# Kernel tuning notes

Hardware: AMD Instinct MI355X
Metric: run time of the kernel (lower is better)

## Reference

```python
import jax, jax.numpy as jnp
import numpy as np

B, C, D, O = 4, 4096, 1024, 1024
PROJ = 256
RANKS = [1, 2, 4, 8]
E = len(RANKS)
CLAMP_MAX = float(np.log(1.0 / 0.01))  # log(100)


def setup_inputs() -> dict:
    key = jax.random.key(0)
    ks = jax.random.split(key, 16)
    inp = {
        "x": jax.random.normal(ks[0], (B, C, D), dtype=jnp.float32),
        "W": jax.random.normal(ks[1], (O, D), dtype=jnp.float32) / np.sqrt(D),
        "Wp": jax.random.normal(ks[2], (PROJ, D), dtype=jnp.float32) / np.sqrt(D),
        "bp": jnp.zeros((PROJ,), dtype=jnp.float32),
        "sim": jax.random.normal(ks[3], (PROJ, E), dtype=jnp.float32) * 0.01,
        "temp": jnp.full((1,), np.log(1.0 / 0.5), dtype=jnp.float32),
    }
    for i, r in enumerate(RANKS):
        inp[f"Wd{i}"] = jax.random.normal(ks[4 + 2 * i], (r, D), dtype=jnp.float32) / r
        inp[f"Wu{i}"] = jax.random.normal(ks[5 + 2 * i], (O, r), dtype=jnp.float32) * 0.01
    return inp


def _l2norm(v, axis):
    return v / jnp.maximum(jnp.linalg.norm(v, axis=axis, keepdims=True), 1e-12)


def reference(x, W, Wp, bp, sim, temp, Wd0, Wu0, Wd1, Wu1, Wd2, Wu2, Wd3, Wu3):
    # base linear (bias=False)
    base = jnp.einsum("bcd,od->bco", x, W)

    # cosine top-k gate on flattened tokens
    xf = x.reshape(-1, x.shape[-1])                         # [N, D]
    proj = _l2norm(xf @ Wp.T + bp, axis=1)                  # [N, PROJ]
    simn = _l2norm(sim, axis=0)                             # [PROJ, E]
    scale = jnp.exp(jnp.minimum(temp, CLAMP_MAX))
    logits = (proj @ simn) * scale                          # [N, E]

    # eval mode: no noise. softmax then top-1 mask * prob
    lw = jax.nn.softmax(logits, axis=1)
    top1 = jnp.argmax(lw, axis=1)                           # [N]
    ret = jnp.where(jnp.arange(E)[None, :] == top1[:, None], lw, 0.0)
    ret = ret.reshape(x.shape[0], x.shape[1], E)            # [B, C, E]

    # dense per-expert LoRA (ranks differ, so small fixed loop)
    downs = (Wd0, Wd1, Wd2, Wd3)
    ups = (Wu0, Wu1, Wu2, Wu3)
    l = jnp.stack(
        [jnp.einsum("bcr,or->bco", jnp.einsum("bcd,rd->bcr", x, d), u)
         for d, u in zip(downs, ups)],
        axis=2,
    )                                                       # [B, C, E, O]
    res = jnp.sum(ret[..., None] * l, axis=2)               # [B, C, O]
    return base + res
```

## Files before the change

### kernel.cpp

```cpp
#include <hip/hip_runtime.h>

#define TOK 16384
#define DD 1024
#define OO 1024
#define KE 1088
#define NT 17
#define NB1 288
#define CLAMPV 4.605170185988091f

typedef __attribute__((ext_vector_type(8))) short short8;
typedef __attribute__((ext_vector_type(4))) float f32x4;

__device__ __forceinline__ unsigned short f2bf(float f) {
  unsigned int u = __float_as_uint(f);
  return (unsigned short)((u + 0x7FFFu + ((u >> 16) & 1u)) >> 16);
}

__device__ __forceinline__ void gload16(const unsigned short* g, unsigned short* l) {
  __builtin_amdgcn_global_load_lds(
      (const __attribute__((address_space(1))) void*)g,
      (__attribute__((address_space(3))) void*)l, 16, 0, 0);
}

__device__ __forceinline__ float down_val(int j, int d,
    const float* __restrict__ Wd0, const float* __restrict__ Wd1,
    const float* __restrict__ Wd2, const float* __restrict__ Wd3) {
  if (j == 0) return Wd0[d];
  if (j < 3) return Wd1[(j - 1) * DD + d];
  if (j < 7) return Wd2[(j - 3) * DD + d];
  if (j < 15) return Wd3[(j - 7) * DD + d];
  return 0.f;
}

__global__ __launch_bounds__(256) void prep3(
    const float* __restrict__ W, const float* __restrict__ Wp,
    const float* __restrict__ sim, const float* __restrict__ bp,
    const float* __restrict__ Wd0, const float* __restrict__ Wd1,
    const float* __restrict__ Wd2, const float* __restrict__ Wd3,
    const float* __restrict__ Wu0, const float* __restrict__ Wu1,
    const float* __restrict__ Wu2, const float* __restrict__ Wu3,
    unsigned short* __restrict__ Bx, unsigned short* __restrict__ B1,
    unsigned short* __restrict__ Ax, float* __restrict__ v4,
    float* __restrict__ c4) {
  __shared__ float simn_l[256][4];
  __shared__ float part[4][4];
  const int tid = threadIdx.x;
  if (blockIdx.x < 4) {
    float4 sv = *(const float4*)&sim[tid * 4];
    float v[4] = {sv.x * sv.x, sv.y * sv.y, sv.z * sv.z, sv.w * sv.w};
#pragma unroll
    for (int off = 1; off < 64; off <<= 1) {
#pragma unroll
      for (int e = 0; e < 4; ++e) v[e] += __shfl_xor(v[e], off, 64);
    }
    int wv = tid >> 6, ln = tid & 63;
    if (ln == 0) { part[wv][0] = v[0]; part[wv][1] = v[1]; part[wv][2] = v[2]; part[wv][3] = v[3]; }
    __syncthreads();
    float n0 = fmaxf(sqrtf(part[0][0] + part[1][0] + part[2][0] + part[3][0]), 1e-12f);
    float n1 = fmaxf(sqrtf(part[0][1] + part[1][1] + part[2][1] + part[3][1]), 1e-12f);
    float n2 = fmaxf(sqrtf(part[0][2] + part[1][2] + part[2][2] + part[3][2]), 1e-12f);
    float n3 = fmaxf(sqrtf(part[0][3] + part[1][3] + part[2][3] + part[3][3]), 1e-12f);
    simn_l[tid][0] = sv.x / n0; simn_l[tid][1] = sv.y / n1;
    simn_l[tid][2] = sv.z / n2; simn_l[tid][3] = sv.w / n3;
    __syncthreads();
    int d = blockIdx.x * 256 + tid;
    float a0 = 0.f, a1 = 0.f, a2 = 0.f, a3 = 0.f;
    for (int j = 0; j < 256; ++j) {
      float w = Wp[j * DD + d];
      a0 = __builtin_fmaf(w, simn_l[j][0], a0);
      a1 = __builtin_fmaf(w, simn_l[j][1], a1);
      a2 = __builtin_fmaf(w, simn_l[j][2], a2);
      a3 = __builtin_fmaf(w, simn_l[j][3], a3);
    }
    v4[d] = a0; v4[1024 + d] = a1; v4[2048 + d] = a2; v4[3072 + d] = a3;
    if (blockIdx.x == 0) {
      float bpv = bp[tid];
      float pc[4] = {simn_l[tid][0] * bpv, simn_l[tid][1] * bpv,
                     simn_l[tid][2] * bpv, simn_l[tid][3] * bpv};
#pragma unroll
      for (int off = 1; off < 64; off <<= 1) {
#pragma unroll
        for (int e = 0; e < 4; ++e) pc[e] += __shfl_xor(pc[e], off, 64);
      }
      __syncthreads();
      if (ln == 0) { part[wv][0] = pc[0]; part[wv][1] = pc[1]; part[wv][2] = pc[2]; part[wv][3] = pc[3]; }
      __syncthreads();
      if (tid == 0) {
#pragma unroll
        for (int e = 0; e < 4; ++e)
          c4[e] = part[0][e] + part[1][e] + part[2][e] + part[3][e];
      }
    }
  }
  const int nB1 = NB1 * DD;
  const int nWb = OO * KE;
  const int nXpad = TOK * 48;
  const int total = nB1 + nWb + nXpad;
  for (int i = blockIdx.x * 256 + tid; i < total; i += gridDim.x * 256) {
    if (i < nB1) {
      int r = i >> 10, c = i & 1023;
      float v = 0.f;
      if (r < 256) v = Wp[r * DD + c];
      else if (r < 271) v = down_val(r - 256, c, Wd0, Wd1, Wd2, Wd3);
      B1[i] = f2bf(v);
    } else if (i < nB1 + nWb) {
      int j = i - nB1;
      int o = j / KE, c = j - o * KE;
      float v = 0.f;
      if (c < 1024) v = W[o * DD + c];
      else if (c == 1024) v = Wu0[o];
      else if (c < 1027) v = Wu1[o * 2 + (c - 1025)];
      else if (c < 1031) v = Wu2[o * 4 + (c - 1027)];
      else if (c < 1039) v = Wu3[o * 8 + (c - 1031)];
      Bx[j] = f2bf(v);
    } else {
      int j = i - nB1 - nWb;
      int row = j / 48, c = j - row * 48;
      Ax[row * KE + 1040 + c] = 0;
    }
  }
}

__global__ __launch_bounds__(256, 2) void gemm2f(
    const float* __restrict__ x, const float* __restrict__ v4,
    unsigned short* __restrict__ Ax, const unsigned short* __restrict__ B1,
    const float* __restrict__ c4, const float* __restrict__ bp,
    const float* __restrict__ temp) {
  __shared__ __align__(16) unsigned short as1[2][32 * 32];
  __shared__ __align__(16) unsigned short bs1[2][NB1 * 32];
  __shared__ float ssq_s[2][32];
  __shared__ float xdown_s[32][16];
  __shared__ __align__(16) float dots_s[32][4];
  const int tid = threadIdx.x;
  const int lane = tid & 63, wv = tid >> 6;
  const int wm = wv >> 1, wn = wv & 1;
  const int r0 = blockIdx.x * 32;
  const int ro = lane & 15, ko = (lane >> 4) * 8;
  const int srow = lane >> 2, scol = (lane & 3) * 8;
  const int xr = tid >> 3;
  const int xc = (tid & 7) * 4;
  const float* xgp = &x[(r0 + xr) * DD + xc];
  unsigned short* axp = &Ax[(r0 + xr) * KE + xc];
  f32x4 acc[9] = {};
  float dotp[4] = {};

#define STB1(KT, BUF)                                                         \
  for (int c = wv; c < 18; c += 4)                                            \
    gload16(&B1[(c * 16 + srow) * DD + (KT) * 32 + scol], &bs1[BUF][c * 512]);

#define XSTG(KT, BUF) do {                                                    \
    float4 xv = *(const float4*)(xgp + (KT) * 32);                            \
    float4 va = *(const float4*)&v4[(KT) * 32 + xc];                          \
    float4 vb = *(const float4*)&v4[1024 + (KT) * 32 + xc];                   \
    float4 vc = *(const float4*)&v4[2048 + (KT) * 32 + xc];                   \
    float4 vd = *(const float4*)&v4[3072 + (KT) * 32 + xc];                   \
    dotp[0] = __builtin_fmaf(xv.x, va.x, __builtin_fmaf(xv.y, va.y,           \
              __builtin_fmaf(xv.z, va.z, __builtin_fmaf(xv.w, va.w, dotp[0])))); \
    dotp[1] = __builtin_fmaf(xv.x, vb.x, __builtin_fmaf(xv.y, vb.y,           \
              __builtin_fmaf(xv.z, vb.z, __builtin_fmaf(xv.w, vb.w, dotp[1])))); \
    dotp[2] = __builtin_fmaf(xv.x, vc.x, __builtin_fmaf(xv.y, vc.y,           \
              __builtin_fmaf(xv.z, vc.z, __builtin_fmaf(xv.w, vc.w, dotp[2])))); \
    dotp[3] = __builtin_fmaf(xv.x, vd.x, __builtin_fmaf(xv.y, vd.y,           \
              __builtin_fmaf(xv.z, vd.z, __builtin_fmaf(xv.w, vd.w, dotp[3])))); \
    union { unsigned short s[4]; uint2 q; } pk;                               \
    pk.s[0] = f2bf(xv.x); pk.s[1] = f2bf(xv.y);                               \
    pk.s[2] = f2bf(xv.z); pk.s[3] = f2bf(xv.w);                               \
    *reinterpret_cast<uint2*>(axp + (KT) * 32) = pk.q;                        \
    *reinterpret_cast<uint2*>(&as1[BUF][xr * 32 + xc]) = pk.q;                \
  } while (0)

#define MM(BUF) do {                                                          \
    const unsigned short* ap = &as1[BUF][0];                                  \
    const unsigned short* bpp = &bs1[BUF][0];                                 \
    short8 af = *reinterpret_cast<const short8*>(ap + (wm * 16 + ro) * 32 + ko); \
    _Pragma("unroll")                                                         \
    for (int n = 0; n < 9; ++n) {                                             \
      short8 bf = *reinterpret_cast<const short8*>(                           \
          bpp + (wn * 144 + n * 16 + ro) * 32 + ko);                          \
      acc[n] = __builtin_amdgcn_mfma_f32_16x16x32_bf16(af, bf, acc[n], 0, 0, 0); \
    }                                                                         \
  } while (0)

  XSTG(0, 0);
  STB1(0, 0)
  __syncthreads();
  int cur = 0;
  for (int u = 0; u < 32; ++u) {
    if (u < 31) {
      XSTG(u + 1, cur ^ 1);
      STB1(u + 1, cur ^ 1)
    }
    MM(cur);
    if (u < 31) {
      __syncthreads();
      cur ^= 1;
    }
  }

#pragma unroll
  for (int off = 1; off < 8; off <<= 1) {
#pragma unroll
    for (int e = 0; e < 4; ++e) dotp[e] += __shfl_xor(dotp[e], off, 64);
  }
  if ((lane & 7) == 0) {
    dots_s[xr][0] = dotp[0]; dots_s[xr][1] = dotp[1];
    dots_s[xr][2] = dotp[2]; dots_s[xr][3] = dotp[3];
  }

  float ssqp[4] = {};
#pragma unroll
  for (int n = 0; n < 9; ++n) {
    int col = wn * 144 + n * 16 + ro;
    if (col < 256) {
      float b = bp[col];
#pragma unroll
      for (int r = 0; r < 4; ++r) {
        float a = acc[n][r] + b;
        ssqp[r] = __builtin_fmaf(a, a, ssqp[r]);
      }
    }
  }
#pragma unroll
  for (int off = 1; off < 16; off <<= 1) {
#pragma unroll
    for (int r = 0; r < 4; ++r) ssqp[r] += __shfl_xor(ssqp[r], off, 64);
  }
  if (ro == 0) {
#pragma unroll
    for (int r = 0; r < 4; ++r)
      ssq_s[wn][wm * 16 + (lane >> 4) * 4 + r] = ssqp[r];
  }
  if (wn == 1 && ro < 15) {
#pragma unroll
    for (int r = 0; r < 4; ++r)
      xdown_s[wm * 16 + (lane >> 4) * 4 + r][ro] = acc[7][r];
  }
  __syncthreads();

  if (tid < 32) {
    const int row = tid, t = r0 + row;
    float ssqT = ssq_s[0][row] + ssq_s[1][row];
    float4 cc = *reinterpret_cast<const float4*>(c4);
    float scale = expf(fminf(temp[0], CLAMPV));
    float inv = scale / fmaxf(sqrtf(ssqT), 1e-12f);
    float l[4];
    l[0] = (dots_s[row][0] + cc.x) * inv; l[1] = (dots_s[row][1] + cc.y) * inv;
    l[2] = (dots_s[row][2] + cc.z) * inv; l[3] = (dots_s[row][3] + cc.w) * inv;
    int be = 0; float m = l[0];
    if (l[1] > m) { m = l[1]; be = 1; }
    if (l[2] > m) { m = l[2]; be = 2; }
    if (l[3] > m) { m = l[3]; be = 3; }
    float den = expf(l[0] - m) + expf(l[1] - m) + expf(l[2] - m) + expf(l[3] - m);
    float g = 1.0f / den;
    int off = (1 << be) - 1;
    int rr = 1 << be;
    union { unsigned short s[16]; uint4 v[2]; } o;
#pragma unroll
    for (int j = 0; j < 16; ++j) {
      float dv = xdown_s[row][j & 15];
      float v = (j >= off && j < off + rr) ? g * dv : 0.f;
      o.s[j] = f2bf(v);
    }
    uint4* dst = reinterpret_cast<uint4*>(&Ax[t * KE + 1024]);
    dst[0] = o.v[0];
    dst[1] = o.v[1];
  }
#undef STB1
#undef XSTG
#undef MM
}

__global__ __launch_bounds__(512, 2) void main_gemm8(
    const unsigned short* __restrict__ A, const unsigned short* __restrict__ Bm,
    float* __restrict__ C) {
  __shared__ __align__(16) unsigned short lbuf[2][32768];
  const int tid = threadIdx.x;
  const int lane = tid & 63, wv = tid >> 6;
  const int wm = wv >> 2, wn = wv & 3;
  const int dd = blockIdx.x;
  const int tt = (dd & 7) * 32 + (dd >> 3);
  const int bx = tt & 3, by = tt >> 2;
  const int r0 = by * 256, c0 = bx * 256;
  const int ro = lane & 15, ko = (lane >> 4) * 8;
  const int rowb = ro * 128;
  const int swz = (ro & 7) << 4;
  const int lk0 = (ko * 2) ^ swz;
  const int lk1 = (64 + ko * 2) ^ swz;
  const int ll = (lane * 16) ^ ((lane >> 3) << 4);
  const int sro = ll >> 7;
  const int sk = (ll & 127) >> 1;
  f32x4 acc[8][4] = {};
  short8 Af[4][2], B0[2][2], B1r[2][2];

#define STG(MTX, GRB, HBU, BUF, U2)                                           \
  do {                                                                        \
    gload16(&MTX[((GRB) + (0 * 8 + wv) * 8 + sro) * KE + (U2) * 64 + sk],     \
            &lbuf[BUF][(HBU) + (0 * 8 + wv) * 512]);                          \
    gload16(&MTX[((GRB) + (1 * 8 + wv) * 8 + sro) * KE + (U2) * 64 + sk],     \
            &lbuf[BUF][(HBU) + (1 * 8 + wv) * 512]);                          \
  } while (0)

#define LDA(FI, QM, LK) (*reinterpret_cast<const short8*>(                    \
    (const char*)Ab + wm * 16384 + (QM) * 8192 + (FI) * 2048 + rowb + (LK)))
#define LDB(FN, QN, LK) (*reinterpret_cast<const short8*>(                    \
    (const char*)Bb + wn * 8192 + (QN) * 4096 + (FN) * 2048 + rowb + (LK)))

#define MMQ(QM, QN, BF)                                                       \
  do {                                                                        \
    _Pragma("unroll")                                                         \
    for (int fi = 0; fi < 4; ++fi) {                                          \
      _Pragma("unroll")                                                       \
      for (int fn = 0; fn < 2; ++fn) {                                        \
        acc[(QM)*4+fi][(QN)*2+fn] = __builtin_amdgcn_mfma_f32_16x16x32_bf16(  \
            Af[fi][0], BF[fn][0], acc[(QM)*4+fi][(QN)*2+fn], 0, 0, 0);        \
        acc[(QM)*4+fi][(QN)*2+fn] = __builtin_amdgcn_mfma_f32_16x16x32_bf16(  \
            Af[fi][1], BF[fn][1], acc[(QM)*4+fi][(QN)*2+fn], 0, 0, 0);        \
      }                                                                       \
    }                                                                         \
  } while (0)

  STG(Bm, c0,       16384, 0, 0);
  STG(A,  r0,       0,     0, 0);
  STG(Bm, c0 + 128, 24576, 0, 0);
  STG(A,  r0 + 128, 8192,  0, 0);
  STG(Bm, c0,       16384, 1, 1);
  STG(A,  r0,       0,     1, 1);
  asm volatile("s_waitcnt vmcnt(4)" ::: "memory");
  __builtin_amdgcn_s_barrier();

  for (int u = 0; u < NT; ++u) {
    const int db = u & 1;
    const unsigned short* Ab = &lbuf[db][0];
    const unsigned short* Bb = &lbuf[db][16384];
#pragma unroll
    for (int fi = 0; fi < 4; ++fi) { Af[fi][0] = LDA(fi, 0, lk0); Af[fi][1] = LDA(fi, 0, lk1); }
#pragma unroll
    for (int fn = 0; fn < 2; ++fn) { B0[fn][0] = LDB(fn, 0, lk0); B0[fn][1] = LDB(fn, 0, lk1); }
    if (u + 1 < NT) STG(Bm, c0 + 128, 24576, (u + 1) & 1, u + 1);
    __builtin_amdgcn_s_barrier();
    __builtin_amdgcn_s_setprio(1);
    MMQ(0, 0, B0);
    __builtin_amdgcn_s_setprio(0);
    __builtin_amdgcn_s_barrier();
#pragma unroll
    for (int fn = 0; fn < 2; ++fn) { B1r[fn][0] = LDB(fn, 1, lk0); B1r[fn][1] = LDB(fn, 1, lk1); }
    if (u + 1 < NT) STG(A, r0 + 128, 8192, (u + 1) & 1, u + 1);
    __builtin_amdgcn_s_barrier();
    __builtin_amdgcn_s_setprio(1);
    MMQ(0, 1, B1r);
    __builtin_amdgcn_s_setprio(0);
    __builtin_amdgcn_s_barrier();
#pragma unroll
    for (int fi = 0; fi < 4; ++fi) { Af[fi][0] = LDA(fi, 1, lk0); Af[fi][1] = LDA(fi, 1, lk1); }
    if (u + 2 < NT) STG(Bm, c0, 16384, db, u + 2);
    __builtin_amdgcn_s_barrier();
    __builtin_amdgcn_s_setprio(1);
    MMQ(1, 1, B1r);
    __builtin_amdgcn_s_setprio(0);
    __builtin_amdgcn_s_barrier();
    if (u + 2 < NT) STG(A, r0, 0, db, u + 2);
    __builtin_amdgcn_s_barrier();
    __builtin_amdgcn_s_setprio(1);
    MMQ(1, 0, B0);
    __builtin_amdgcn_s_setprio(0);
    if (u + 2 < NT) {
      asm volatile("s_waitcnt vmcnt(4)" ::: "memory");
    } else if (u == NT - 2) {
      asm volatile("s_waitcnt vmcnt(0)" ::: "memory");
    }
    __builtin_amdgcn_s_barrier();
  }

#pragma unroll
  for (int m = 0; m < 8; ++m) {
    int rr = r0 + wm * 128 + m * 16 + (lane >> 4) * 4;
#pragma unroll
    for (int n = 0; n < 4; ++n) {
      int cc = c0 + wn * 64 + n * 16 + ro;
#pragma unroll
      for (int v = 0; v < 4; ++v)
        C[(rr + v) * OO + cc] = acc[m][n][v];
    }
  }
#undef STG
#undef LDA
#undef LDB
#undef MMQ
}

extern "C" void kernel_launch(void* const* d_in, const int* in_sizes, int n_in,
                              void* d_out, int out_size, void* d_ws, size_t ws_size,
                              hipStream_t stream) {
  const float* x    = (const float*)d_in[0];
  const float* W    = (const float*)d_in[1];
  const float* Wp   = (const float*)d_in[2];
  const float* bp   = (const float*)d_in[3];
  const float* sim  = (const float*)d_in[4];
  const float* temp = (const float*)d_in[5];
  const float* Wd0  = (const float*)d_in[6];
  const float* Wu0  = (const float*)d_in[7];
  const float* Wd1  = (const float*)d_in[8];
  const float* Wu1  = (const float*)d_in[9];
  const float* Wd2  = (const float*)d_in[10];
  const float* Wu2  = (const float*)d_in[11];
  const float* Wd3  = (const float*)d_in[12];
  const float* Wu3  = (const float*)d_in[13];
  float* out = (float*)d_out;
  char* ws = (char*)d_ws;
  unsigned short* Ax  = (unsigned short*)ws;
  unsigned short* Bx  = (unsigned short*)(ws + 35651584);
  unsigned short* B1  = (unsigned short*)(ws + 37879808);
  float* v4           = (float*)(ws + 38469632);
  float* c4           = (float*)(ws + 38486016);

  prep3<<<1024, 256, 0, stream>>>(W, Wp, sim, bp, Wd0, Wd1, Wd2, Wd3,
                                  Wu0, Wu1, Wu2, Wu3, Bx, B1, Ax, v4, c4);
  gemm2f<<<512, 256, 0, stream>>>(x, v4, Ax, B1, c4, bp, temp);
  main_gemm8<<<256, 512, 0, stream>>>(Ax, Bx, out);
}
```

Baseline: 107.4 us.

## Pre-tile and XOR-swizzle gate weights, double the gate GEMM K-step to 64

prep3 now writes B1 in a K-tiled layout of 64-wide slices with an XOR swizzle on the k index, so gemm2f can stage each tile with contiguous 16-byte LDS loads. The gate GEMM k-step grows from 32 to 64, halving the number of pipeline iterations and barriers, and LDS reads use the matching swizzle to avoid bank conflicts. The epilogue scratch arrays now alias the B tile buffer to offset the larger LDS footprint. The cost is more LDS per block, which may reduce occupancy at two blocks per CU.

Measured after the change: 98.01 us. -8.7%, faster.

```diff
diff --git a/kernel.cpp b/kernel.cpp
--- a/kernel.cpp
+++ b/kernel.cpp
@@ -92,16 +92,19 @@
       }
     }
   }
-  const int nB1 = NB1 * DD;
+  const int nB1 = 16 * NB1 * 64;
   const int nWb = OO * KE;
   const int nXpad = TOK * 48;
   const int total = nB1 + nWb + nXpad;
   for (int i = blockIdx.x * 256 + tid; i < total; i += gridDim.x * 256) {
     if (i < nB1) {
-      int r = i >> 10, c = i & 1023;
+      int kt = i / (NB1 * 64);
+      int rem = i - kt * (NB1 * 64);
+      int r = rem >> 6, kk = rem & 63;
+      int k = kt * 64 + (kk ^ ((r & 7) << 3));
       float v = 0.f;
-      if (r < 256) v = Wp[r * DD + c];
-      else if (r < 271) v = down_val(r - 256, c, Wd0, Wd1, Wd2, Wd3);
+      if (r < 256) v = Wp[r * DD + k];
+      else if (r < 271) v = down_val(r - 256, k, Wd0, Wd1, Wd2, Wd3);
       B1[i] = f2bf(v);
     } else if (i < nB1 + nWb) {
       int j = i - nB1;
@@ -123,37 +126,37 @@
 
 __global__ __launch_bounds__(256, 2) void gemm2f(
     const float* __restrict__ x, const float* __restrict__ v4,
-    unsigned short* __restrict__ Ax, const unsigned short* __restrict__ B1,
+    unsigned short* __restrict__ Ax, const unsigned short* __restrict__ B1L,
     const float* __restrict__ c4, const float* __restrict__ bp,
     const float* __restrict__ temp) {
-  __shared__ __align__(16) unsigned short as1[2][32 * 32];
-  __shared__ __align__(16) unsigned short bs1[2][NB1 * 32];
-  __shared__ float ssq_s[2][32];
-  __shared__ float xdown_s[32][16];
-  __shared__ __align__(16) float dots_s[32][4];
+  __shared__ __align__(16) unsigned short as1[2][32 * 64];
+  __shared__ __align__(16) unsigned short bs1[2][NB1 * 64];
   const int tid = threadIdx.x;
   const int lane = tid & 63, wv = tid >> 6;
   const int wm = wv >> 1, wn = wv & 1;
   const int r0 = blockIdx.x * 32;
-  const int ro = lane & 15, ko = (lane >> 4) * 8;
-  const int srow = lane >> 2, scol = (lane & 3) * 8;
+  const int ro = lane & 15;
+  const int rswz = (ro & 7) << 3;
   const int xr = tid >> 3;
   const int xc = (tid & 7) * 4;
+  const int aswz = (xr & 7) << 3;
   const float* xgp = &x[(r0 + xr) * DD + xc];
   unsigned short* axp = &Ax[(r0 + xr) * KE + xc];
   f32x4 acc[9] = {};
   float dotp[4] = {};
 
 #define STB1(KT, BUF)                                                         \
-  for (int c = wv; c < 18; c += 4)                                            \
-    gload16(&B1[(c * 16 + srow) * DD + (KT) * 32 + scol], &bs1[BUF][c * 512]);
-
-#define XSTG(KT, BUF) do {                                                    \
-    float4 xv = *(const float4*)(xgp + (KT) * 32);                            \
-    float4 va = *(const float4*)&v4[(KT) * 32 + xc];                          \
-    float4 vb = *(const float4*)&v4[1024 + (KT) * 32 + xc];                   \
-    float4 vc = *(const float4*)&v4[2048 + (KT) * 32 + xc];                   \
-    float4 vd = *(const float4*)&v4[3072 + (KT) * 32 + xc];                   \
+  for (int c = wv; c < 36; c += 4)                                            \
+    gload16(&B1L[(KT) * (NB1 * 64) + c * 512 + lane * 8], &bs1[BUF][c * 512]);
+
+#define XSTG(KT, BUF)                                                         \
+  _Pragma("unroll")                                                           \
+  for (int h = 0; h < 2; ++h) {                                               \
+    float4 xv = *(const float4*)(xgp + (KT) * 64 + h * 32);                   \
+    float4 va = *(const float4*)&v4[(KT) * 64 + h * 32 + xc];                 \
+    float4 vb = *(const float4*)&v4[1024 + (KT) * 64 + h * 32 + xc];          \
+    float4 vc = *(const float4*)&v4[2048 + (KT) * 64 + h * 32 + xc];          \
+    float4 vd = *(const float4*)&v4[3072 + (KT) * 64 + h * 32 + xc];          \
     dotp[0] = __builtin_fmaf(xv.x, va.x, __builtin_fmaf(xv.y, va.y,           \
               __builtin_fmaf(xv.z, va.z, __builtin_fmaf(xv.w, va.w, dotp[0])))); \
     dotp[1] = __builtin_fmaf(xv.x, vb.x, __builtin_fmaf(xv.y, vb.y,           \
@@ -165,37 +168,46 @@
     union { unsigned short s[4]; uint2 q; } pk;                               \
     pk.s[0] = f2bf(xv.x); pk.s[1] = f2bf(xv.y);                               \
     pk.s[2] = f2bf(xv.z); pk.s[3] = f2bf(xv.w);                               \
-    *reinterpret_cast<uint2*>(axp + (KT) * 32) = pk.q;                        \
-    *reinterpret_cast<uint2*>(&as1[BUF][xr * 32 + xc]) = pk.q;                \
-  } while (0)
-
-#define MM(BUF) do {                                                          \
-    const unsigned short* ap = &as1[BUF][0];                                  \
-    const unsigned short* bpp = &bs1[BUF][0];                                 \
-    short8 af = *reinterpret_cast<const short8*>(ap + (wm * 16 + ro) * 32 + ko); \
+    *reinterpret_cast<uint2*>(axp + (KT) * 64 + h * 32) = pk.q;               \
+    *reinterpret_cast<uint2*>(                                                \
+        &as1[BUF][xr * 64 + (((h << 5) + xc) ^ aswz)]) = pk.q;                \
+  }
+
+#define MM(BUF)                                                               \
+  _Pragma("unroll")                                                           \
+  for (int kh = 0; kh < 2; ++kh) {                                            \
+    const int kb = ((kh << 5) + ((lane >> 4) << 3)) ^ rswz;                   \
+    short8 af = *reinterpret_cast<const short8*>(                             \
+        &as1[BUF][(wm * 16 + ro) * 64 + kb]);                                 \
     _Pragma("unroll")                                                         \
     for (int n = 0; n < 9; ++n) {                                             \
       short8 bf = *reinterpret_cast<const short8*>(                           \
-          bpp + (wn * 144 + n * 16 + ro) * 32 + ko);                          \
+          &bs1[BUF][(wn * 144 + n * 16 + ro) * 64 + kb]);                     \
       acc[n] = __builtin_amdgcn_mfma_f32_16x16x32_bf16(af, bf, acc[n], 0, 0, 0); \
     }                                                                         \
-  } while (0)
-
-  XSTG(0, 0);
+  }
+
   STB1(0, 0)
+  XSTG(0, 0)
   __syncthreads();
   int cur = 0;
-  for (int u = 0; u < 32; ++u) {
-    if (u < 31) {
-      XSTG(u + 1, cur ^ 1);
+  for (int u = 0; u < 16; ++u) {
+    if (u < 15) {
       STB1(u + 1, cur ^ 1)
-    }
-    MM(cur);
-    if (u < 31) {
+      XSTG(u + 1, cur ^ 1)
+    }
+    MM(cur)
+    if (u < 15) {
       __syncthreads();
       cur ^= 1;
     }
   }
+  __syncthreads();
+
+  float* eps = (float*)&bs1[0][0];
+  float* ssq_s = eps;
+  float* xdown_s = eps + 64;
+  float* dots_s = eps + 576;
 
 #pragma unroll
   for (int off = 1; off < 8; off <<= 1) {
@@ -203,8 +215,8 @@
     for (int e = 0; e < 4; ++e) dotp[e] += __shfl_xor(dotp[e], off, 64);
   }
   if ((lane & 7) == 0) {
-    dots_s[xr][0] = dotp[0]; dots_s[xr][1] = dotp[1];
-    dots_s[xr][2] = dotp[2]; dots_s[xr][3] = dotp[3];
+    dots_s[xr * 4 + 0] = dotp[0]; dots_s[xr * 4 + 1] = dotp[1];
+    dots_s[xr * 4 + 2] = dotp[2]; dots_s[xr * 4 + 3] = dotp[3];
   }
 
   float ssqp[4] = {};
@@ -228,24 +240,24 @@
   if (ro == 0) {
 #pragma unroll
     for (int r = 0; r < 4; ++r)
-      ssq_s[wn][wm * 16 + (lane >> 4) * 4 + r] = ssqp[r];
+      ssq_s[wn * 32 + wm * 16 + (lane >> 4) * 4 + r] = ssqp[r];
   }
   if (wn == 1 && ro < 15) {
 #pragma unroll
     for (int r = 0; r < 4; ++r)
-      xdown_s[wm * 16 + (lane >> 4) * 4 + r][ro] = acc[7][r];
+      xdown_s[(wm * 16 + (lane >> 4) * 4 + r) * 16 + ro] = acc[7][r];
   }
   __syncthreads();
 
   if (tid < 32) {
     const int row = tid, t = r0 + row;
-    float ssqT = ssq_s[0][row] + ssq_s[1][row];
+    float ssqT = ssq_s[row] + ssq_s[32 + row];
     float4 cc = *reinterpret_cast<const float4*>(c4);
     float scale = expf(fminf(temp[0], CLAMPV));
     float inv = scale / fmaxf(sqrtf(ssqT), 1e-12f);
     float l[4];
-    l[0] = (dots_s[row][0] + cc.x) * inv; l[1] = (dots_s[row][1] + cc.y) * inv;
-    l[2] = (dots_s[row][2] + cc.z) * inv; l[3] = (dots_s[row][3] + cc.w) * inv;
+    l[0] = (dots_s[row * 4 + 0] + cc.x) * inv; l[1] = (dots_s[row * 4 + 1] + cc.y) * inv;
+    l[2] = (dots_s[row * 4 + 2] + cc.z) * inv; l[3] = (dots_s[row * 4 + 3] + cc.w) * inv;
     int be = 0; float m = l[0];
     if (l[1] > m) { m = l[1]; be = 1; }
     if (l[2] > m) { m = l[2]; be = 2; }
@@ -257,7 +269,7 @@
     union { unsigned short s[16]; uint4 v[2]; } o;
 #pragma unroll
     for (int j = 0; j < 16; ++j) {
-      float dv = xdown_s[row][j & 15];
+      float dv = xdown_s[row * 16 + (j & 15)];
       float v = (j >= off && j < off + rr) ? g * dv : 0.f;
       o.s[j] = f2bf(v);
     }
@@ -409,12 +421,12 @@
   char* ws = (char*)d_ws;
   unsigned short* Ax  = (unsigned short*)ws;
   unsigned short* Bx  = (unsigned short*)(ws + 35651584);
-  unsigned short* B1  = (unsigned short*)(ws + 37879808);
+  unsigned short* B1L = (unsigned short*)(ws + 37879808);
   float* v4           = (float*)(ws + 38469632);
   float* c4           = (float*)(ws + 38486016);
 
   prep3<<<1024, 256, 0, stream>>>(W, Wp, sim, bp, Wd0, Wd1, Wd2, Wd3,
-                                  Wu0, Wu1, Wu2, Wu3, Bx, B1, Ax, v4, c4);
-  gemm2f<<<512, 256, 0, stream>>>(x, v4, Ax, B1, c4, bp, temp);
+                                  Wu0, Wu1, Wu2, Wu3, Bx, B1L, Ax, v4, c4);
+  gemm2f<<<512, 256, 0, stream>>>(x, v4, Ax, B1L, c4, bp, temp);
   main_gemm8<<<256, 512, 0, stream>>>(Ax, Bx, out);
 }
```

## Drop LDS staging in gate GEMM; load MFMA fragments directly from global

Applied to the files above, without the earlier changes.

The gate/projection GEMM kernel no longer stages the x tile and B1 tile through double-buffered shared memory with barriers. Each wave now reads its MFMA A fragments straight from fp32 x (converting to bf16 in registers) and its B fragments straight from global B1, with the K loop stepping 64 at a time. This removes LDS traffic and __syncthreads. In exchange, x is read redundantly from global/L2, B fragments are uncoalesced strided global loads, and there is no explicit prefetch overlap.

New measurement: 169.3 us. +57.7%, slower.

```diff
diff --git a/kernel.cpp b/kernel.cpp
--- a/kernel.cpp
+++ b/kernel.cpp
@@ -121,13 +121,11 @@
   }
 }
 
-__global__ __launch_bounds__(256, 2) void gemm2f(
+__global__ __launch_bounds__(256, 2) void gemm3f(
     const float* __restrict__ x, const float* __restrict__ v4,
     unsigned short* __restrict__ Ax, const unsigned short* __restrict__ B1,
     const float* __restrict__ c4, const float* __restrict__ bp,
     const float* __restrict__ temp) {
-  __shared__ __align__(16) unsigned short as1[2][32 * 32];
-  __shared__ __align__(16) unsigned short bs1[2][NB1 * 32];
   __shared__ float ssq_s[2][32];
   __shared__ float xdown_s[32][16];
   __shared__ __align__(16) float dots_s[32][4];
@@ -135,65 +133,50 @@
   const int lane = tid & 63, wv = tid >> 6;
   const int wm = wv >> 1, wn = wv & 1;
   const int r0 = blockIdx.x * 32;
-  const int ro = lane & 15, ko = (lane >> 4) * 8;
-  const int srow = lane >> 2, scol = (lane & 3) * 8;
+  const int ro = lane & 15;
+  const int ko = (lane >> 4) * 8;
   const int xr = tid >> 3;
   const int xc = (tid & 7) * 4;
   const float* xgp = &x[(r0 + xr) * DD + xc];
   unsigned short* axp = &Ax[(r0 + xr) * KE + xc];
+  const float* xfp = &x[(r0 + wm * 16 + ro) * DD + ko];
+  const unsigned short* bfp = &B1[(wn * 144 + ro) * DD + ko];
   f32x4 acc[9] = {};
   float dotp[4] = {};
 
-#define STB1(KT, BUF)                                                         \
-  for (int c = wv; c < 18; c += 4)                                            \
-    gload16(&B1[(c * 16 + srow) * DD + (KT) * 32 + scol], &bs1[BUF][c * 512]);
-
-#define XSTG(KT, BUF) do {                                                    \
-    float4 xv = *(const float4*)(xgp + (KT) * 32);                            \
-    float4 va = *(const float4*)&v4[(KT) * 32 + xc];                          \
-    float4 vb = *(const float4*)&v4[1024 + (KT) * 32 + xc];                   \
-    float4 vc = *(const float4*)&v4[2048 + (KT) * 32 + xc];                   \
-    float4 vd = *(const float4*)&v4[3072 + (KT) * 32 + xc];                   \
-    dotp[0] = __builtin_fmaf(xv.x, va.x, __builtin_fmaf(xv.y, va.y,           \
-              __builtin_fmaf(xv.z, va.z, __builtin_fmaf(xv.w, va.w, dotp[0])))); \
-    dotp[1] = __builtin_fmaf(xv.x, vb.x, __builtin_fmaf(xv.y, vb.y,           \
-              __builtin_fmaf(xv.z, vb.z, __builtin_fmaf(xv.w, vb.w, dotp[1])))); \
-    dotp[2] = __builtin_fmaf(xv.x, vc.x, __builtin_fmaf(xv.y, vc.y,           \
-              __builtin_fmaf(xv.z, vc.z, __builtin_fmaf(xv.w, vc.w, dotp[2])))); \
-    dotp[3] = __builtin_fmaf(xv.x, vd.x, __builtin_fmaf(xv.y, vd.y,           \
-              __builtin_fmaf(xv.z, vd.z, __builtin_fmaf(xv.w, vd.w, dotp[3])))); \
-    union { unsigned short s[4]; uint2 q; } pk;                               \
-    pk.s[0] = f2bf(xv.x); pk.s[1] = f2bf(xv.y);                               \
-    pk.s[2] = f2bf(xv.z); pk.s[3] = f2bf(xv.w);                               \
-    *reinterpret_cast<uint2*>(axp + (KT) * 32) = pk.q;                        \
-    *reinterpret_cast<uint2*>(&as1[BUF][xr * 32 + xc]) = pk.q;                \
-  } while (0)
-
-#define MM(BUF) do {                                                          \
-    const unsigned short* ap = &as1[BUF][0];                                  \
-    const unsigned short* bpp = &bs1[BUF][0];                                 \
-    short8 af = *reinterpret_cast<const short8*>(ap + (wm * 16 + ro) * 32 + ko); \
-    _Pragma("unroll")                                                         \
-    for (int n = 0; n < 9; ++n) {                                             \
-      short8 bf = *reinterpret_cast<const short8*>(                           \
-          bpp + (wn * 144 + n * 16 + ro) * 32 + ko);                          \
-      acc[n] = __builtin_amdgcn_mfma_f32_16x16x32_bf16(af, bf, acc[n], 0, 0, 0); \
-    }                                                                         \
-  } while (0)
-
-  XSTG(0, 0);
-  STB1(0, 0)
-  __syncthreads();
-  int cur = 0;
-  for (int u = 0; u < 32; ++u) {
-    if (u < 31) {
-      XSTG(u + 1, cur ^ 1);
-      STB1(u + 1, cur ^ 1)
-    }
-    MM(cur);
-    if (u < 31) {
-      __syncthreads();
-      cur ^= 1;
+  for (int u = 0; u < 16; ++u) {
+#pragma unroll
+    for (int h = 0; h < 2; ++h) {
+      float4 xv = *(const float4*)(xgp + u * 64 + h * 32);
+      float4 va = *(const float4*)&v4[u * 64 + h * 32 + xc];
+      float4 vb = *(const float4*)&v4[1024 + u * 64 + h * 32 + xc];
+      float4 vc = *(const float4*)&v4[2048 + u * 64 + h * 32 + xc];
+      float4 vd = *(const float4*)&v4[3072 + u * 64 + h * 32 + xc];
+      dotp[0] = __builtin_fmaf(xv.x, va.x, __builtin_fmaf(xv.y, va.y,
+                __builtin_fmaf(xv.z, va.z, __builtin_fmaf(xv.w, va.w, dotp[0]))));
+      dotp[1] = __builtin_fmaf(xv.x, vb.x, __builtin_fmaf(xv.y, vb.y,
+                __builtin_fmaf(xv.z, vb.z, __builtin_fmaf(xv.w, vb.w, dotp[1]))));
+      dotp[2] = __builtin_fmaf(xv.x, vc.x, __builtin_fmaf(xv.y, vc.y,
+                __builtin_fmaf(xv.z, vc.z, __builtin_fmaf(xv.w, vc.w, dotp[2]))));
+      dotp[3] = __builtin_fmaf(xv.x, vd.x, __builtin_fmaf(xv.y, vd.y,
+                __builtin_fmaf(xv.z, vd.z, __builtin_fmaf(xv.w, vd.w, dotp[3]))));
+      union { unsigned short s[4]; uint2 q; } pk;
+      pk.s[0] = f2bf(xv.x); pk.s[1] = f2bf(xv.y);
+      pk.s[2] = f2bf(xv.z); pk.s[3] = f2bf(xv.w);
+      *reinterpret_cast<uint2*>(axp + u * 64 + h * 32) = pk.q;
+    }
+#pragma unroll
+    for (int kh = 0; kh < 2; ++kh) {
+      float4 a0 = *(const float4*)(xfp + u * 64 + kh * 32);
+      float4 a1 = *(const float4*)(xfp + u * 64 + kh * 32 + 4);
+      union { unsigned short s[8]; short8 v; } af;
+      af.s[0] = f2bf(a0.x); af.s[1] = f2bf(a0.y); af.s[2] = f2bf(a0.z); af.s[3] = f2bf(a0.w);
+      af.s[4] = f2bf(a1.x); af.s[5] = f2bf(a1.y); af.s[6] = f2bf(a1.z); af.s[7] = f2bf(a1.w);
+#pragma unroll
+      for (int n = 0; n < 9; ++n) {
+        short8 bf = *reinterpret_cast<const short8*>(bfp + n * 16 * DD + u * 64 + kh * 32);
+        acc[n] = __builtin_amdgcn_mfma_f32_16x16x32_bf16(af.v, bf, acc[n], 0, 0, 0);
+      }
     }
   }
 
@@ -265,9 +248,6 @@
     dst[0] = o.v[0];
     dst[1] = o.v[1];
   }
-#undef STB1
-#undef XSTG
-#undef MM
 }
 
 __global__ __launch_bounds__(512, 2) void main_gemm8(
@@ -415,6 +395,6 @@
 
   prep3<<<1024, 256, 0, stream>>>(W, Wp, sim, bp, Wd0, Wd1, Wd2, Wd3,
                                   Wu0, Wu1, Wu2, Wu3, Bx, B1, Ax, v4, c4);
-  gemm2f<<<512, 256, 0, stream>>>(x, v4, Ax, B1, c4, bp, temp);
+  gemm3f<<<512, 256, 0, stream>>>(x, v4, Ax, B1, c4, bp, temp);
   main_gemm8<<<256, 512, 0, stream>>>(Ax, Bx, out);
 }
```
